# Kernel tuning notes

Hardware: AMD Instinct MI355X
Metric: run time of the kernel (lower is better)

The kernel has to match this reference:

```python
import jax, jax.numpy as jnp
import numpy as np

NEG_SLOPE = 0.2  # PyG GATConv default


def gat_conv(h, src, dst, n_nodes, W, a_src, a_dst, bias, concat):
    """PyG-style GATConv (single linear shared across src/dst, self-loops
    already included in src/dst). W: [heads*out, in]; a_*: [heads, out]."""
    heads, out = a_src.shape
    g = (h @ W.T).reshape(-1, heads, out)  # [N, H, D]
    # per-node attention logits, then gather scalars per edge (PyG order)
    al_src = jnp.einsum('nhd,hd->nh', g, a_src)  # [N, H]
    al_dst = jnp.einsum('nhd,hd->nh', g, a_dst)
    e = jax.nn.leaky_relu(al_src[src] + al_dst[dst], NEG_SLOPE)  # [E, H]
    # segment softmax over incoming edges of each dst node
    e_max = jax.ops.segment_max(e, dst, num_segments=n_nodes)
    e_exp = jnp.exp(e - e_max[dst])
    denom = jax.ops.segment_sum(e_exp, dst, num_segments=n_nodes)
    alpha = e_exp / denom[dst]  # every node has a self-loop -> denom > 0
    msg = g[src] * alpha[..., None]  # [E, H, D]
    out_n = jax.ops.segment_sum(msg, dst, num_segments=n_nodes)  # [N, H, D]
    if concat:
        out_n = out_n.reshape(n_nodes, heads * out)
    else:
        out_n = out_n.mean(axis=1)
    return out_n + bias


def setup_inputs() -> dict:
    key = jax.random.key(0)
    ks = jax.random.split(key, 20)
    N, M = 100000, 1600000
    node_dim, edge_dim, global_dim = 12, 5, 11
    hidden, heads, num_targets = 32, 4, 4
    in1 = node_dim + global_dim  # 23
    s = 0.1
    inp = {
        'x': jax.random.normal(ks[0], (N, node_dim), jnp.float32),
        'edge_index': jax.random.randint(ks[1], (2, M), 0, N, jnp.int32),
        'edge_attr': jax.random.normal(ks[2], (M, edge_dim), jnp.float32),
        'u': jax.random.normal(ks[3], (1, global_dim), jnp.float32),
        # conv1: in1 -> hidden per head, concat
        'W1': jax.random.normal(ks[4], (heads * hidden, in1), jnp.float32) * s,
        'a_src1': jax.random.normal(ks[5], (heads, hidden), jnp.float32) * s,
        'a_dst1': jax.random.normal(ks[6], (heads, hidden), jnp.float32) * s,
        'b1': jnp.zeros((heads * hidden,), jnp.float32),
        # conv2: heads*hidden -> hidden, mean over heads
        'W2': jax.random.normal(ks[7], (heads * hidden, heads * hidden), jnp.float32) * s,
        'a_src2': jax.random.normal(ks[8], (heads, hidden), jnp.float32) * s,
        'a_dst2': jax.random.normal(ks[9], (heads, hidden), jnp.float32) * s,
        'b2': jnp.zeros((hidden,), jnp.float32),
        # decoder: (2*hidden + edge_dim) -> 2*hidden -> hidden -> num_targets
        'dw1': jax.random.normal(ks[10], (2 * hidden, 2 * hidden + edge_dim), jnp.float32) * s,
        'db1': jnp.zeros((2 * hidden,), jnp.float32),
        'dw2': jax.random.normal(ks[11], (hidden, 2 * hidden), jnp.float32) * s,
        'db2': jnp.zeros((hidden,), jnp.float32),
        'dw3': jax.random.normal(ks[12], (num_targets, hidden), jnp.float32) * s,
        'db3': jnp.zeros((num_targets,), jnp.float32),
    }
    return inp


def reference(x, edge_index, edge_attr, u, W1, a_src1, a_dst1, b1,
              W2, a_src2, a_dst2, b2, dw1, db1, dw2, db2, dw3, db3):
    N = x.shape[0]
    loop = jnp.arange(N, dtype=edge_index.dtype)
    src = jnp.concatenate([edge_index[0], loop])  # add self-loops (PyG default)
    dst = jnp.concatenate([edge_index[1], loop])

    u_node = jnp.broadcast_to(u, (N, u.shape[-1]))
    h = jnp.concatenate([x, u_node], axis=-1)  # [N, 23]

    h = jax.nn.elu(gat_conv(h, src, dst, N, W1, a_src1, a_dst1, b1, True))
    h = jax.nn.elu(gat_conv(h, src, dst, N, W2, a_src2, a_dst2, b2, False))

    s0, d0 = edge_index[0], edge_index[1]
    e_in = jnp.concatenate([h[s0], h[d0], edge_attr], axis=-1)  # [M, 69]
    z = jax.nn.relu(e_in @ dw1.T + db1)
    z = jax.nn.relu(z @ dw2.T + db2)
    return z @ dw3.T + db3  # [M, num_targets]
```

## Files before the change

kernel.cpp:

```cpp
#include <hip/hip_runtime.h>

#define DEVINL __device__ __forceinline__

DEVINL float leakyf(float v) { return v > 0.f ? v : 0.2f * v; }
DEVINL float eluf(float v)   { return v > 0.f ? v : __expf(v) - 1.f; }

__global__ void __launch_bounds__(256) k_izero(int* __restrict__ p, int total) {
  int t = blockIdx.x * blockDim.x + threadIdx.x;
  if (t < total) p[t] = 0;
}

__global__ void __launch_bounds__(256) k_count(const int* __restrict__ ei,
                                               int* __restrict__ cnt, int M, int E) {
  int e = blockIdx.x * blockDim.x + threadIdx.x;
  if (e >= E) return;
  int d = (e < M) ? ei[M + e] : e - M;
  atomicAdd(&cnt[d], 1);
}

__global__ void __launch_bounds__(256) k_scan1(const int* __restrict__ cnt,
                                               int* __restrict__ off,
                                               int* __restrict__ bsum, int N) {
  __shared__ int sh[256];
  int i = blockIdx.x * 256 + threadIdx.x;
  int v = (i < N) ? cnt[i] : 0;
  sh[threadIdx.x] = v;
  __syncthreads();
  for (int o = 1; o < 256; o <<= 1) {
    int t = (threadIdx.x >= o) ? sh[threadIdx.x - o] : 0;
    __syncthreads();
    sh[threadIdx.x] += t;
    __syncthreads();
  }
  if (i < N) off[i] = sh[threadIdx.x] - v;
  if (threadIdx.x == 255) bsum[blockIdx.x] = sh[255];
}

__global__ void __launch_bounds__(512) k_scan2(int* __restrict__ bsum, int nb) {
  __shared__ int sh[512];
  int t = threadIdx.x;
  int v = (t < nb) ? bsum[t] : 0;
  sh[t] = v;
  __syncthreads();
  for (int o = 1; o < 512; o <<= 1) {
    int x = (t >= o) ? sh[t - o] : 0;
    __syncthreads();
    sh[t] += x;
    __syncthreads();
  }
  if (t < nb) bsum[t] = sh[t] - v;
}

__global__ void __launch_bounds__(256) k_scan3(int* __restrict__ off,
                                               const int* __restrict__ bsum,
                                               int* __restrict__ cur, int N, int E) {
  int i = blockIdx.x * 256 + threadIdx.x;
  if (i < N) { off[i] += bsum[i >> 8]; cur[i] = 0; }
  if (i == N) off[N] = E;
}

__global__ void __launch_bounds__(256) k_fill(const int* __restrict__ ei,
                                              const int* __restrict__ off,
                                              int* __restrict__ cur,
                                              int* __restrict__ ssrc,
                                              int* __restrict__ idst,
                                              int* __restrict__ ieid, int M, int E) {
  int e = blockIdx.x * blockDim.x + threadIdx.x;
  if (e >= E) return;
  int s, d, id;
  if (e < M) { s = ei[e]; d = ei[M + e]; id = e; }
  else       { s = e - M; d = s; id = -1; }
  int pos = off[d] + atomicAdd(&cur[d], 1);
  ssrc[pos] = s;
  idst[pos] = d;
  ieid[pos] = id;
}

__global__ void k_prep(const float* __restrict__ W1, const float* __restrict__ as1,
                       const float* __restrict__ ad1,
                       const float* __restrict__ W2, const float* __restrict__ as2,
                       const float* __restrict__ ad2,
                       float* __restrict__ wa1s, float* __restrict__ wa1d,
                       float* __restrict__ wa2s, float* __restrict__ wa2d) {
  int t = threadIdx.x;
  if (t < 92) {
    int h = t / 23, c = t % 23;
    float s1 = 0.f, s2 = 0.f;
    for (int dd = 0; dd < 32; ++dd) {
      float w = W1[(h * 32 + dd) * 23 + c];
      s1 += w * as1[h * 32 + dd];
      s2 += w * ad1[h * 32 + dd];
    }
    wa1s[t] = s1;
    wa1d[t] = s2;
  }
  {
    int h = t >> 7, c = t & 127;
    float s1 = 0.f, s2 = 0.f;
    for (int dd = 0; dd < 32; ++dd) {
      float w = W2[(h * 32 + dd) * 128 + c];
      s1 += w * as2[h * 32 + dd];
      s2 += w * ad2[h * 32 + dd];
    }
    wa2s[t] = s1;
    wa2d[t] = s2;
  }
}

__global__ void __launch_bounds__(128) k_g1(
    const float* __restrict__ x, const float* __restrict__ u,
    const float* __restrict__ W1,
    const float* __restrict__ wa1s, const float* __restrict__ wa1d,
    float* __restrict__ g1, float* __restrict__ al1s, float* __restrict__ al1d) {
  int n = blockIdx.x, k = threadIdx.x;
  __shared__ float hs[23];
  if (k < 12) hs[k] = x[n * 12 + k];
  else if (k < 23) hs[k] = u[k - 12];
  __syncthreads();
  const float* w = W1 + k * 23;
  float s = 0.f;
#pragma unroll
  for (int c = 0; c < 23; ++c) s += hs[c] * w[c];
  g1[n * 128 + k] = s;
  if (k < 8) {
    int h = k & 3;
    const float* wa = (k < 4 ? wa1s : wa1d) + h * 23;
    float t = 0.f;
#pragma unroll
    for (int c = 0; c < 23; ++c) t += hs[c] * wa[c];
    (k < 4 ? al1s : al1d)[n * 4 + h] = t;
  }
}

template <int MODE>
__global__ void __launch_bounds__(256) k_gat(
    const float* __restrict__ g, const float* __restrict__ als,
    const float* __restrict__ ald, const int* __restrict__ off,
    const int* __restrict__ ssrc, const float* __restrict__ bias,
    float* __restrict__ outp, int N) {
  int wid = threadIdx.x >> 6, lane = threadIdx.x & 63;
  int d = blockIdx.x * 4 + wid;
  if (d >= N) return;
  int h = lane >> 4;
  float av = ald[d * 4 + h];
  int p0 = off[d], p1 = off[d + 1];
  float accx = 0.f, accy = 0.f, den = 0.f;
  int p = p0;
  for (; p + 4 <= p1; p += 4) {
    int s0 = ssrc[p], s1 = ssrc[p + 1], s2 = ssrc[p + 2], s3 = ssrc[p + 3];
    float l0 = als[s0 * 4 + h], l1 = als[s1 * 4 + h];
    float l2 = als[s2 * 4 + h], l3 = als[s3 * 4 + h];
    float2 G0 = *(const float2*)(g + (size_t)s0 * 128 + 2 * lane);
    float2 G1 = *(const float2*)(g + (size_t)s1 * 128 + 2 * lane);
    float2 G2 = *(const float2*)(g + (size_t)s2 * 128 + 2 * lane);
    float2 G3 = *(const float2*)(g + (size_t)s3 * 128 + 2 * lane);
    float w0 = __expf(leakyf(l0 + av)), w1 = __expf(leakyf(l1 + av));
    float w2 = __expf(leakyf(l2 + av)), w3 = __expf(leakyf(l3 + av));
    accx += w0 * G0.x + w1 * G1.x + w2 * G2.x + w3 * G3.x;
    accy += w0 * G0.y + w1 * G1.y + w2 * G2.y + w3 * G3.y;
    den += (w0 + w1) + (w2 + w3);
  }
  for (; p < p1; ++p) {
    int s = ssrc[p];
    float w = __expf(leakyf(als[s * 4 + h] + av));
    float2 G = *(const float2*)(g + (size_t)s * 128 + 2 * lane);
    accx += w * G.x;
    accy += w * G.y;
    den += w;
  }
  float inv = 1.f / den;
  float vx = accx * inv, vy = accy * inv;
  if (MODE == 0) {
    float2 b = *(const float2*)(bias + 2 * lane);
    float2 o;
    o.x = eluf(vx + b.x);
    o.y = eluf(vy + b.y);
    *(float2*)(outp + (size_t)d * 128 + 2 * lane) = o;
  } else {
    float sx = vx + __shfl_xor(vx, 16);
    sx += __shfl_xor(sx, 32);
    float sy = vy + __shfl_xor(vy, 16);
    sy += __shfl_xor(sy, 32);
    if (lane < 16) {
      float2 o;
      o.x = eluf(0.25f * sx + bias[2 * lane]);
      o.y = eluf(0.25f * sy + bias[2 * lane + 1]);
      *(float2*)(outp + (size_t)d * 32 + 2 * lane) = o;
    }
  }
}

__global__ void __launch_bounds__(128) k_g2t(
    const float* __restrict__ h2, const float* __restrict__ W2,
    const float* __restrict__ wa2s, const float* __restrict__ wa2d,
    float* __restrict__ g2, float* __restrict__ al2s, float* __restrict__ al2d,
    int N, int ntiles) {
  __shared__ float4 w4s[128][32];
  __shared__ float4 hs4[32][32];
  int t = threadIdx.x;

  for (int i = t; i < 4096; i += 128) {
    int c = i >> 5, kk = i & 31;
    float4 v = *(const float4*)(W2 + c * 128 + kk * 4);
    w4s[c][kk ^ ((c >> 2) & 31)] = v;
  }

  int m = t & 31, grp = t >> 5;
  int c0 = 4 * m;

  for (int tile = blockIdx.x; tile < ntiles; tile += gridDim.x) {
    int n0 = tile * 32;
    __syncthreads();
    for (int i = t; i < 1024; i += 128) {
      int n = i >> 5, kk = i & 31;
      int nn = n0 + n;
      hs4[n][kk] = (nn < N) ? *(const float4*)(h2 + (size_t)nn * 128 + kk * 4)
                            : make_float4(0.f, 0.f, 0.f, 0.f);
    }
    __syncthreads();

    float acc[8][4];
#pragma unroll
    for (int n = 0; n < 8; ++n)
#pragma unroll
      for (int j = 0; j < 4; ++j) acc[n][j] = 0.f;

#pragma unroll 8
    for (int kk = 0; kk < 32; ++kk) {
      float4 wj[4];
#pragma unroll
      for (int j = 0; j < 4; ++j) wj[j] = w4s[c0 + j][kk ^ m];
#pragma unroll
      for (int n = 0; n < 8; ++n) {
        float4 hv = hs4[grp * 8 + n][kk];
#pragma unroll
        for (int j = 0; j < 4; ++j) {
          acc[n][j] += hv.x * wj[j].x + hv.y * wj[j].y +
                       hv.z * wj[j].z + hv.w * wj[j].w;
        }
      }
    }
#pragma unroll
    for (int n = 0; n < 8; ++n) {
      int nn = n0 + grp * 8 + n;
      if (nn < N)
        *(float4*)(g2 + (size_t)nn * 128 + c0) =
            make_float4(acc[n][0], acc[n][1], acc[n][2], acc[n][3]);
    }

    for (int v = 0; v < 2; ++v) {
      int idx = t + 128 * v;
      int n = idx >> 3, j = idx & 7, h = j & 3;
      int nn = n0 + n;
      if (nn < N) {
        const float4* wa = (const float4*)((j < 4 ? wa2s : wa2d) + h * 128);
        float s = 0.f;
#pragma unroll
        for (int kk = 0; kk < 32; ++kk) {
          float4 a = hs4[n][kk];
          float4 w = wa[kk];
          s += a.x * w.x + a.y * w.y + a.z * w.z + a.w * w.w;
        }
        (j < 4 ? al2s : al2d)[(size_t)nn * 4 + h] = s;
      }
    }
  }
}

__global__ void __launch_bounds__(256) k_pq(
    const float* __restrict__ h3, const float* __restrict__ dw1,
    float* __restrict__ pq, int N) {
  __shared__ float4 ws4[64][16];
  __shared__ float ht[64][32];
  int t = threadIdx.x;
  for (int i = t; i < 4096; i += 256) {
    int k = i >> 6, c = i & 63;
    ((float*)&ws4[k][(c >> 2) ^ (k & 15)])[c & 3] = dw1[k * 69 + c];
  }
  int n0 = blockIdx.x * 64;
  for (int i = t; i < 2048; i += 256) {
    int n = i >> 5, c = i & 31;
    int nn = n0 + n;
    ht[n][c] = (nn < N) ? h3[(size_t)nn * 32 + c] : 0.f;
  }
  __syncthreads();
  int k2 = t & 127, sub = t >> 7;
  int k = k2 & 63, base4 = (k2 < 64) ? 0 : 8;
  float4 wr[8];
#pragma unroll
  for (int i = 0; i < 8; ++i) wr[i] = ws4[k][(base4 + i) ^ (k & 15)];
  for (int ii = 0; ii < 32; ++ii) {
    int n = sub * 32 + ii;
    const float4* hr = (const float4*)ht[n];
    float s = 0.f;
#pragma unroll
    for (int i = 0; i < 8; ++i) {
      float4 a = hr[i], w = wr[i];
      s += a.x * w.x + a.y * w.y + a.z * w.z + a.w * w.w;
    }
    int nn = n0 + n;
    if (nn < N) pq[(size_t)nn * 128 + k2] = s;
  }
}

__global__ void __launch_bounds__(256) k_dec(
    const float* __restrict__ pq, const int* __restrict__ ssrc,
    const int* __restrict__ idst, const int* __restrict__ ieid,
    const float* __restrict__ ea,
    const float* __restrict__ dw1, const float* __restrict__ db1,
    const float* __restrict__ dw2, const float* __restrict__ db2,
    const float* __restrict__ dw3, const float* __restrict__ db3,
    float* __restrict__ out, int E) {
  __shared__ float4 w2s4[32][16];
  __shared__ float4 ct4[5][16];
  __shared__ float4 b1q[16];
  __shared__ float4 b2q[8];
  __shared__ float4 w3s4[4][8];
  __shared__ float  db3s[4];
  int t = threadIdx.x;
  for (int i = t; i < 512; i += 256) {
    int k = i >> 4, cq = i & 15;
    w2s4[k][cq] = *(const float4*)(dw2 + k * 64 + cq * 4);
  }
  if (t < 80) {
    int c = t / 16, cq = t % 16;
    float4 v;
    v.x = dw1[(4 * cq + 0) * 69 + 64 + c];
    v.y = dw1[(4 * cq + 1) * 69 + 64 + c];
    v.z = dw1[(4 * cq + 2) * 69 + 64 + c];
    v.w = dw1[(4 * cq + 3) * 69 + 64 + c];
    ct4[c][cq] = v;
  } else if (t < 96) {
    b1q[t - 80] = *(const float4*)(db1 + 4 * (t - 80));
  } else if (t < 104) {
    b2q[t - 96] = *(const float4*)(db2 + 4 * (t - 96));
  } else if (t < 136) {
    int o = (t - 104) >> 3, cq = (t - 104) & 7;
    w3s4[o][cq] = *(const float4*)(dw3 + o * 32 + 4 * cq);
  } else if (t < 140) {
    db3s[t - 136] = db3[t - 136];
  }
  __syncthreads();

  int pos0 = blockIdx.x * 512 + t;
  int pos1 = pos0 + 256;
  bool okA = pos0 < E, okB = pos1 < E;
  int pa = okA ? pos0 : 0, pb = okB ? pos1 : 0;
  int eA_ = okA ? ieid[pa] : -1;
  int eB_ = okB ? ieid[pb] : -1;
  bool wA = eA_ >= 0, wB = eB_ >= 0;
  int eidA = wA ? eA_ : 0, eidB = wB ? eB_ : 0;
  int sA = ssrc[pa], dA = idst[pa];
  int sB = ssrc[pb], dB = idst[pb];
  const float4* PA = (const float4*)(pq + (size_t)sA * 128);
  const float4* QA = (const float4*)(pq + (size_t)dA * 128 + 64);
  const float4* PB = (const float4*)(pq + (size_t)sB * 128);
  const float4* QB = (const float4*)(pq + (size_t)dB * 128 + 64);
  const float* eap = ea + (size_t)eidA * 5;
  const float* ebp = ea + (size_t)eidB * 5;
  float eAv[5], eBv[5];
#pragma unroll
  for (int c = 0; c < 5; ++c) { eAv[c] = eap[c]; eBv[c] = ebp[c]; }

  float z2a[32], z2b[32];
#pragma unroll
  for (int kq = 0; kq < 8; ++kq) {
    float4 b = b2q[kq];
    z2a[4 * kq + 0] = b.x; z2a[4 * kq + 1] = b.y;
    z2a[4 * kq + 2] = b.z; z2a[4 * kq + 3] = b.w;
    z2b[4 * kq + 0] = b.x; z2b[4 * kq + 1] = b.y;
    z2b[4 * kq + 2] = b.z; z2b[4 * kq + 3] = b.w;
  }

  for (int cq = 0; cq < 16; ++cq) {
    float4 pA = PA[cq], qA = QA[cq];
    float4 pB = PB[cq], qB = QB[cq];
    float4 bq = b1q[cq];
    float4 zA, zB;
    zA.x = pA.x + qA.x + bq.x; zA.y = pA.y + qA.y + bq.y;
    zA.z = pA.z + qA.z + bq.z; zA.w = pA.w + qA.w + bq.w;
    zB.x = pB.x + qB.x + bq.x; zB.y = pB.y + qB.y + bq.y;
    zB.z = pB.z + qB.z + bq.z; zB.w = pB.w + qB.w + bq.w;
#pragma unroll
    for (int c = 0; c < 5; ++c) {
      float4 cc = ct4[c][cq];
      float ca = eAv[c], cb = eBv[c];
      zA.x += ca * cc.x; zA.y += ca * cc.y; zA.z += ca * cc.z; zA.w += ca * cc.w;
      zB.x += cb * cc.x; zB.y += cb * cc.y; zB.z += cb * cc.z; zB.w += cb * cc.w;
    }
    zA.x = fmaxf(zA.x, 0.f); zA.y = fmaxf(zA.y, 0.f);
    zA.z = fmaxf(zA.z, 0.f); zA.w = fmaxf(zA.w, 0.f);
    zB.x = fmaxf(zB.x, 0.f); zB.y = fmaxf(zB.y, 0.f);
    zB.z = fmaxf(zB.z, 0.f); zB.w = fmaxf(zB.w, 0.f);
#pragma unroll
    for (int k = 0; k < 32; ++k) {
      float4 w = w2s4[k][cq];
      z2a[k] += w.x * zA.x + w.y * zA.y + w.z * zA.z + w.w * zA.w;
      z2b[k] += w.x * zB.x + w.y * zB.y + w.z * zB.z + w.w * zB.w;
    }
  }
#pragma unroll
  for (int k = 0; k < 32; ++k) {
    z2a[k] = fmaxf(z2a[k], 0.f);
    z2b[k] = fmaxf(z2b[k], 0.f);
  }

  float oA[4], oB[4];
#pragma unroll
  for (int o = 0; o < 4; ++o) { oA[o] = db3s[o]; oB[o] = db3s[o]; }
#pragma unroll
  for (int cq = 0; cq < 8; ++cq) {
    float ax = z2a[4 * cq], ay = z2a[4 * cq + 1];
    float az = z2a[4 * cq + 2], aw = z2a[4 * cq + 3];
    float bx = z2b[4 * cq], by = z2b[4 * cq + 1];
    float bz = z2b[4 * cq + 2], bw = z2b[4 * cq + 3];
#pragma unroll
    for (int o = 0; o < 4; ++o) {
      float4 w = w3s4[o][cq];
      oA[o] += ax * w.x + ay * w.y + az * w.z + aw * w.w;
      oB[o] += bx * w.x + by * w.y + bz * w.z + bw * w.w;
    }
  }
  if (wA && okA)
    *(float4*)(out + (size_t)eidA * 4) = make_float4(oA[0], oA[1], oA[2], oA[3]);
  if (wB && okB)
    *(float4*)(out + (size_t)eidB * 4) = make_float4(oB[0], oB[1], oB[2], oB[3]);
}

extern "C" void kernel_launch(void* const* d_in, const int* in_sizes, int n_in,
                              void* d_out, int out_size, void* d_ws, size_t ws_size,
                              hipStream_t stream) {
  const float* x   = (const float*)d_in[0];
  const int*   ei  = (const int*)d_in[1];
  const float* ea  = (const float*)d_in[2];
  const float* u   = (const float*)d_in[3];
  const float* W1  = (const float*)d_in[4];
  const float* as1 = (const float*)d_in[5];
  const float* ad1 = (const float*)d_in[6];
  const float* b1  = (const float*)d_in[7];
  const float* W2  = (const float*)d_in[8];
  const float* as2 = (const float*)d_in[9];
  const float* ad2 = (const float*)d_in[10];
  const float* b2  = (const float*)d_in[11];
  const float* dw1 = (const float*)d_in[12];
  const float* db1 = (const float*)d_in[13];
  const float* dw2 = (const float*)d_in[14];
  const float* db2 = (const float*)d_in[15];
  const float* dw3 = (const float*)d_in[16];
  const float* db3 = (const float*)d_in[17];
  float* out = (float*)d_out;

  const int N = in_sizes[0] / 12;
  const int M = in_sizes[1] / 2;
  const int E = M + N;

  float* ws = (float*)d_ws;
  float* A    = ws;
  float* B    = A + (size_t)N * 128;
  float* H3   = B;
  float* AL1S = B + (size_t)N * 128;
  float* AL1D = AL1S + (size_t)N * 4;
  float* AL2S = AL1D + (size_t)N * 4;
  float* AL2D = AL2S + (size_t)N * 4;
  float* WA1S = AL2D + (size_t)N * 4;
  float* WA1D = WA1S + 96;
  float* WA2S = WA1D + 96;
  float* WA2D = WA2S + 512;
  int* IOFF = (int*)(WA2D + 512);
  int* ICUR = IOFF + (N + 1);
  int* IBS  = ICUR + N;
  int* ISRC = IBS + 512;
  int* IDST = ISRC + E;
  int* IEID = IDST + E;

  int nb = (N + 255) / 256;
  int gE = (E + 255) / 256;

  k_izero<<<nb, 256, 0, stream>>>(ICUR, N);
  k_count<<<gE, 256, 0, stream>>>(ei, ICUR, M, E);
  k_scan1<<<nb, 256, 0, stream>>>(ICUR, IOFF, IBS, N);
  k_scan2<<<1, 512, 0, stream>>>(IBS, nb);
  k_scan3<<<(N + 256) / 256, 256, 0, stream>>>(IOFF, IBS, ICUR, N, E);
  k_fill<<<gE, 256, 0, stream>>>(ei, IOFF, ICUR, ISRC, IDST, IEID, M, E);

  k_prep<<<1, 512, 0, stream>>>(W1, as1, ad1, W2, as2, ad2, WA1S, WA1D, WA2S, WA2D);

  k_g1<<<N, 128, 0, stream>>>(x, u, W1, WA1S, WA1D, A, AL1S, AL1D);
  k_gat<0><<<(N + 3) / 4, 256, 0, stream>>>(A, AL1S, AL1D, IOFF, ISRC, b1, B, N);

  int ntiles = (N + 31) / 32;
  k_g2t<<<512, 128, 0, stream>>>(B, W2, WA2S, WA2D, A, AL2S, AL2D, N, ntiles);
  k_gat<1><<<(N + 3) / 4, 256, 0, stream>>>(A, AL2S, AL2D, IOFF, ISRC, b2, H3, N);

  k_pq<<<(N + 63) / 64, 256, 0, stream>>>(H3, dw1, A, N);
  k_dec<<<(E + 511) / 512, 256, 0, stream>>>(A, ISRC, IDST, IEID, ea, dw1, db1,
                                             dw2, db2, dw3, db3, out, E);
}
```

Before: 1.080 ms.

## Compute source-side decoder projection per edge instead of precomputing per node

The per-node precompute now stores only the destination-side projection (64 floats per node) instead of both source and destination halves. The decoder kernel gathers the raw 32-float source embedding and multiplies it by the first 32 columns of dw1, held in shared memory, for each edge. This halves the random-gather bytes for the source side and the precompute write size. In exchange it adds about 2K FMAs per edge pair plus extra registers, which may lower occupancy.

```diff
diff --git a/kernel.cpp b/kernel.cpp
--- a/kernel.cpp
+++ b/kernel.cpp
@@ -267,15 +267,16 @@
   }
 }
 
-__global__ void __launch_bounds__(256) k_pq(
+__global__ void __launch_bounds__(256) k_q(
     const float* __restrict__ h3, const float* __restrict__ dw1,
-    float* __restrict__ pq, int N) {
-  __shared__ float4 ws4[64][16];
+    float* __restrict__ qt, int N) {
+  __shared__ float4 ws4[64][8];
   __shared__ float ht[64][32];
   int t = threadIdx.x;
-  for (int i = t; i < 4096; i += 256) {
-    int k = i >> 6, c = i & 63;
-    ((float*)&ws4[k][(c >> 2) ^ (k & 15)])[c & 3] = dw1[k * 69 + c];
+  for (int i = t; i < 512; i += 256) {
+    int k = i >> 3, q = i & 7;
+    const float* wp = dw1 + k * 69 + 32 + 4 * q;
+    ws4[k][q] = make_float4(wp[0], wp[1], wp[2], wp[3]);
   }
   int n0 = blockIdx.x * 64;
   for (int i = t; i < 2048; i += 256) {
@@ -284,13 +285,12 @@
     ht[n][c] = (nn < N) ? h3[(size_t)nn * 32 + c] : 0.f;
   }
   __syncthreads();
-  int k2 = t & 127, sub = t >> 7;
-  int k = k2 & 63, base4 = (k2 < 64) ? 0 : 8;
+  int k = t & 63, sub = t >> 6;
   float4 wr[8];
 #pragma unroll
-  for (int i = 0; i < 8; ++i) wr[i] = ws4[k][(base4 + i) ^ (k & 15)];
-  for (int ii = 0; ii < 32; ++ii) {
-    int n = sub * 32 + ii;
+  for (int i = 0; i < 8; ++i) wr[i] = ws4[k][i];
+  for (int ii = 0; ii < 16; ++ii) {
+    int n = sub * 16 + ii;
     const float4* hr = (const float4*)ht[n];
     float s = 0.f;
 #pragma unroll
@@ -299,25 +299,35 @@
       s += a.x * w.x + a.y * w.y + a.z * w.z + a.w * w.w;
     }
     int nn = n0 + n;
-    if (nn < N) pq[(size_t)nn * 128 + k2] = s;
+    if (nn < N) qt[(size_t)nn * 64 + k] = s;
   }
 }
 
 __global__ void __launch_bounds__(256) k_dec(
-    const float* __restrict__ pq, const int* __restrict__ ssrc,
-    const int* __restrict__ idst, const int* __restrict__ ieid,
-    const float* __restrict__ ea,
+    const float* __restrict__ h3, const float* __restrict__ qt,
+    const int* __restrict__ ssrc, const int* __restrict__ idst,
+    const int* __restrict__ ieid, const float* __restrict__ ea,
     const float* __restrict__ dw1, const float* __restrict__ db1,
     const float* __restrict__ dw2, const float* __restrict__ db2,
     const float* __restrict__ dw3, const float* __restrict__ db3,
     float* __restrict__ out, int E) {
+  __shared__ float4 at4[32][16];
+  __shared__ float4 ct4[5][16];
   __shared__ float4 w2s4[32][16];
-  __shared__ float4 ct4[5][16];
   __shared__ float4 b1q[16];
   __shared__ float4 b2q[8];
   __shared__ float4 w3s4[4][8];
   __shared__ float  db3s[4];
   int t = threadIdx.x;
+  for (int i = t; i < 512; i += 256) {
+    int c = i >> 4, cq = i & 15;
+    float4 v;
+    v.x = dw1[(4 * cq + 0) * 69 + c];
+    v.y = dw1[(4 * cq + 1) * 69 + c];
+    v.z = dw1[(4 * cq + 2) * 69 + c];
+    v.w = dw1[(4 * cq + 3) * 69 + c];
+    at4[c][cq] = v;
+  }
   for (int i = t; i < 512; i += 256) {
     int k = i >> 4, cq = i & 15;
     w2s4[k][cq] = *(const float4*)(dw2 + k * 64 + cq * 4);
@@ -352,10 +362,22 @@
   int eidA = wA ? eA_ : 0, eidB = wB ? eB_ : 0;
   int sA = ssrc[pa], dA = idst[pa];
   int sB = ssrc[pb], dB = idst[pb];
-  const float4* PA = (const float4*)(pq + (size_t)sA * 128);
-  const float4* QA = (const float4*)(pq + (size_t)dA * 128 + 64);
-  const float4* PB = (const float4*)(pq + (size_t)sB * 128);
-  const float4* QB = (const float4*)(pq + (size_t)dB * 128 + 64);
+
+  float ha[32], hb[32];
+  {
+    const float4* HA = (const float4*)(h3 + (size_t)sA * 32);
+    const float4* HB = (const float4*)(h3 + (size_t)sB * 32);
+#pragma unroll
+    for (int i = 0; i < 8; ++i) {
+      float4 a = HA[i], b = HB[i];
+      ha[4 * i + 0] = a.x; ha[4 * i + 1] = a.y;
+      ha[4 * i + 2] = a.z; ha[4 * i + 3] = a.w;
+      hb[4 * i + 0] = b.x; hb[4 * i + 1] = b.y;
+      hb[4 * i + 2] = b.z; hb[4 * i + 3] = b.w;
+    }
+  }
+  const float4* QA = (const float4*)(qt + (size_t)dA * 64);
+  const float4* QB = (const float4*)(qt + (size_t)dB * 64);
   const float* eap = ea + (size_t)eidA * 5;
   const float* ebp = ea + (size_t)eidB * 5;
   float eAv[5], eBv[5];
@@ -373,14 +395,20 @@
   }
 
   for (int cq = 0; cq < 16; ++cq) {
-    float4 pA = PA[cq], qA = QA[cq];
-    float4 pB = PB[cq], qB = QB[cq];
+    float4 qA = QA[cq], qB = QB[cq];
     float4 bq = b1q[cq];
     float4 zA, zB;
-    zA.x = pA.x + qA.x + bq.x; zA.y = pA.y + qA.y + bq.y;
-    zA.z = pA.z + qA.z + bq.z; zA.w = pA.w + qA.w + bq.w;
-    zB.x = pB.x + qB.x + bq.x; zB.y = pB.y + qB.y + bq.y;
-    zB.z = pB.z + qB.z + bq.z; zB.w = pB.w + qB.w + bq.w;
+    zA.x = qA.x + bq.x; zA.y = qA.y + bq.y;
+    zA.z = qA.z + bq.z; zA.w = qA.w + bq.w;
+    zB.x = qB.x + bq.x; zB.y = qB.y + bq.y;
+    zB.z = qB.z + bq.z; zB.w = qB.w + bq.w;
+#pragma unroll
+    for (int c = 0; c < 32; ++c) {
+      float4 ac = at4[c][cq];
+      float xa = ha[c], xb = hb[c];
+      zA.x += xa * ac.x; zA.y += xa * ac.y; zA.z += xa * ac.z; zA.w += xa * ac.w;
+      zB.x += xb * ac.x; zB.y += xb * ac.y; zB.z += xb * ac.z; zB.w += xb * ac.w;
+    }
 #pragma unroll
     for (int c = 0; c < 5; ++c) {
       float4 cc = ct4[c][cq];
@@ -492,7 +520,8 @@
   k_g2t<<<512, 128, 0, stream>>>(B, W2, WA2S, WA2D, A, AL2S, AL2D, N, ntiles);
   k_gat<1><<<(N + 3) / 4, 256, 0, stream>>>(A, AL2S, AL2D, IOFF, ISRC, b2, H3, N);
 
-  k_pq<<<(N + 63) / 64, 256, 0, stream>>>(H3, dw1, A, N);
-  k_dec<<<(E + 511) / 512, 256, 0, stream>>>(A, ISRC, IDST, IEID, ea, dw1, db1,
-                                             dw2, db2, dw3, db3, out, E);
-}
+  k_q<<<(N + 63) / 64, 256, 0, stream>>>(H3, dw1, A, N);
+  k_dec<<<(E + 511) / 512, 256, 0, stream>>>(H3, A, ISRC, IDST, IEID, ea,
+                                             dw1, db1, dw2, db2, dw3, db3,
+                                             out, E);
+}
```

Result: slower. 1.137 ms (+5.3%).

## Remap edge decoder to half-wavefront per edge with persistent grid

Applied to the files above, without the earlier changes.

The edge MLP decoder moves from one thread per edge (two edges per thread, with 32-wide accumulators in registers) to 32 lanes per edge. Each lane owns one hidden unit of the second layer and keeps its weight row in registers. The first-layer activations go through shared memory, and the final 4-output projection is reduced with xor shuffles. The launch becomes a fixed 2048-block grid-stride loop. The aim is to coalesce the gathered P/Q row reads and cut per-thread register pressure. The cost is shuffle reductions, extra shared-memory traffic, and only one lane in 32 doing the output store.

```diff
diff --git a/kernel.cpp b/kernel.cpp
--- a/kernel.cpp
+++ b/kernel.cpp
@@ -310,121 +310,70 @@
     const float* __restrict__ dw1, const float* __restrict__ db1,
     const float* __restrict__ dw2, const float* __restrict__ db2,
     const float* __restrict__ dw3, const float* __restrict__ db3,
-    float* __restrict__ out, int E) {
-  __shared__ float4 w2s4[32][16];
-  __shared__ float4 ct4[5][16];
-  __shared__ float4 b1q[16];
-  __shared__ float4 b2q[8];
-  __shared__ float4 w3s4[4][8];
-  __shared__ float  db3s[4];
-  int t = threadIdx.x;
-  for (int i = t; i < 512; i += 256) {
-    int k = i >> 4, cq = i & 15;
-    w2s4[k][cq] = *(const float4*)(dw2 + k * 64 + cq * 4);
-  }
-  if (t < 80) {
-    int c = t / 16, cq = t % 16;
-    float4 v;
-    v.x = dw1[(4 * cq + 0) * 69 + 64 + c];
-    v.y = dw1[(4 * cq + 1) * 69 + 64 + c];
-    v.z = dw1[(4 * cq + 2) * 69 + 64 + c];
-    v.w = dw1[(4 * cq + 3) * 69 + 64 + c];
-    ct4[c][cq] = v;
-  } else if (t < 96) {
-    b1q[t - 80] = *(const float4*)(db1 + 4 * (t - 80));
-  } else if (t < 104) {
-    b2q[t - 96] = *(const float4*)(db2 + 4 * (t - 96));
-  } else if (t < 136) {
-    int o = (t - 104) >> 3, cq = (t - 104) & 7;
-    w3s4[o][cq] = *(const float4*)(dw3 + o * 32 + 4 * cq);
-  } else if (t < 140) {
-    db3s[t - 136] = db3[t - 136];
-  }
-  __syncthreads();
-
-  int pos0 = blockIdx.x * 512 + t;
-  int pos1 = pos0 + 256;
-  bool okA = pos0 < E, okB = pos1 < E;
-  int pa = okA ? pos0 : 0, pb = okB ? pos1 : 0;
-  int eA_ = okA ? ieid[pa] : -1;
-  int eB_ = okB ? ieid[pb] : -1;
-  bool wA = eA_ >= 0, wB = eB_ >= 0;
-  int eidA = wA ? eA_ : 0, eidB = wB ? eB_ : 0;
-  int sA = ssrc[pa], dA = idst[pa];
-  int sB = ssrc[pb], dB = idst[pb];
-  const float4* PA = (const float4*)(pq + (size_t)sA * 128);
-  const float4* QA = (const float4*)(pq + (size_t)dA * 128 + 64);
-  const float4* PB = (const float4*)(pq + (size_t)sB * 128);
-  const float4* QB = (const float4*)(pq + (size_t)dB * 128 + 64);
-  const float* eap = ea + (size_t)eidA * 5;
-  const float* ebp = ea + (size_t)eidB * 5;
-  float eAv[5], eBv[5];
-#pragma unroll
-  for (int c = 0; c < 5; ++c) { eAv[c] = eap[c]; eBv[c] = ebp[c]; }
-
-  float z2a[32], z2b[32];
-#pragma unroll
-  for (int kq = 0; kq < 8; ++kq) {
-    float4 b = b2q[kq];
-    z2a[4 * kq + 0] = b.x; z2a[4 * kq + 1] = b.y;
-    z2a[4 * kq + 2] = b.z; z2a[4 * kq + 3] = b.w;
-    z2b[4 * kq + 0] = b.x; z2b[4 * kq + 1] = b.y;
-    z2b[4 * kq + 2] = b.z; z2b[4 * kq + 3] = b.w;
-  }
-
-  for (int cq = 0; cq < 16; ++cq) {
-    float4 pA = PA[cq], qA = QA[cq];
-    float4 pB = PB[cq], qB = QB[cq];
-    float4 bq = b1q[cq];
-    float4 zA, zB;
-    zA.x = pA.x + qA.x + bq.x; zA.y = pA.y + qA.y + bq.y;
-    zA.z = pA.z + qA.z + bq.z; zA.w = pA.w + qA.w + bq.w;
-    zB.x = pB.x + qB.x + bq.x; zB.y = pB.y + qB.y + bq.y;
-    zB.z = pB.z + qB.z + bq.z; zB.w = pB.w + qB.w + bq.w;
-#pragma unroll
-    for (int c = 0; c < 5; ++c) {
-      float4 cc = ct4[c][cq];
-      float ca = eAv[c], cb = eBv[c];
-      zA.x += ca * cc.x; zA.y += ca * cc.y; zA.z += ca * cc.z; zA.w += ca * cc.w;
-      zB.x += cb * cc.x; zB.y += cb * cc.y; zB.z += cb * cc.z; zB.w += cb * cc.w;
-    }
-    zA.x = fmaxf(zA.x, 0.f); zA.y = fmaxf(zA.y, 0.f);
-    zA.z = fmaxf(zA.z, 0.f); zA.w = fmaxf(zA.w, 0.f);
-    zB.x = fmaxf(zB.x, 0.f); zB.y = fmaxf(zB.y, 0.f);
-    zB.z = fmaxf(zB.z, 0.f); zB.w = fmaxf(zB.w, 0.f);
-#pragma unroll
-    for (int k = 0; k < 32; ++k) {
-      float4 w = w2s4[k][cq];
-      z2a[k] += w.x * zA.x + w.y * zA.y + w.z * zA.z + w.w * zA.w;
-      z2b[k] += w.x * zB.x + w.y * zB.y + w.z * zB.z + w.w * zB.w;
-    }
-  }
-#pragma unroll
-  for (int k = 0; k < 32; ++k) {
-    z2a[k] = fmaxf(z2a[k], 0.f);
-    z2b[k] = fmaxf(z2b[k], 0.f);
-  }
-
-  float oA[4], oB[4];
-#pragma unroll
-  for (int o = 0; o < 4; ++o) { oA[o] = db3s[o]; oB[o] = db3s[o]; }
-#pragma unroll
-  for (int cq = 0; cq < 8; ++cq) {
-    float ax = z2a[4 * cq], ay = z2a[4 * cq + 1];
-    float az = z2a[4 * cq + 2], aw = z2a[4 * cq + 3];
-    float bx = z2b[4 * cq], by = z2b[4 * cq + 1];
-    float bz = z2b[4 * cq + 2], bw = z2b[4 * cq + 3];
-#pragma unroll
-    for (int o = 0; o < 4; ++o) {
-      float4 w = w3s4[o][cq];
-      oA[o] += ax * w.x + ay * w.y + az * w.z + aw * w.w;
-      oB[o] += bx * w.x + by * w.y + bz * w.z + bw * w.w;
-    }
-  }
-  if (wA && okA)
-    *(float4*)(out + (size_t)eidA * 4) = make_float4(oA[0], oA[1], oA[2], oA[3]);
-  if (wB && okB)
-    *(float4*)(out + (size_t)eidB * 4) = make_float4(oB[0], oB[1], oB[2], oB[3]);
+    float* __restrict__ out, int E, int npairs) {
+  __shared__ float z1s[4][128];
+  int wv = threadIdx.x >> 6, lane = threadIdx.x & 63;
+  int half = lane >> 5;
+  int k = lane & 31;
+
+  float4 wrow[16];
+#pragma unroll
+  for (int i = 0; i < 16; ++i)
+    wrow[i] = *(const float4*)(dw2 + k * 64 + 4 * i);
+  float w3r0 = dw3[k], w3r1 = dw3[32 + k], w3r2 = dw3[64 + k], w3r3 = dw3[96 + k];
+  float b1a = db1[2 * k], b1b = db1[2 * k + 1];
+  float ct0a = dw1[(2 * k) * 69 + 64], ct0b = dw1[(2 * k + 1) * 69 + 64];
+  float ct1a = dw1[(2 * k) * 69 + 65], ct1b = dw1[(2 * k + 1) * 69 + 65];
+  float ct2a = dw1[(2 * k) * 69 + 66], ct2b = dw1[(2 * k + 1) * 69 + 66];
+  float ct3a = dw1[(2 * k) * 69 + 67], ct3b = dw1[(2 * k + 1) * 69 + 67];
+  float ct4a = dw1[(2 * k) * 69 + 68], ct4b = dw1[(2 * k + 1) * 69 + 68];
+  float b2k = db2[k];
+  float d30 = db3[0], d31 = db3[1], d32 = db3[2], d33 = db3[3];
+
+  float* zme = &z1s[wv][half * 64];
+
+  int stride = gridDim.x * 4;
+  for (int pr = blockIdx.x * 4 + wv; pr < npairs; pr += stride) {
+    int pos = pr * 2 + half;
+    bool ok = pos < E;
+    int pp = ok ? pos : 0;
+    int eid = ok ? ieid[pp] : -1;
+    int s = ssrc[pp], d = idst[pp];
+
+    float2 Pv = *(const float2*)(pq + (size_t)s * 128 + 2 * k);
+    float2 Qv = *(const float2*)(pq + (size_t)d * 128 + 64 + 2 * k);
+    const float* ep = ea + (size_t)(eid < 0 ? 0 : eid) * 5;
+    float e0 = ep[0], e1 = ep[1], e2 = ep[2], e3 = ep[3], e4 = ep[4];
+
+    float za = Pv.x + Qv.x + b1a +
+               ct0a * e0 + ct1a * e1 + ct2a * e2 + ct3a * e3 + ct4a * e4;
+    float zb = Pv.y + Qv.y + b1b +
+               ct0b * e0 + ct1b * e1 + ct2b * e2 + ct3b * e3 + ct4b * e4;
+    za = fmaxf(za, 0.f);
+    zb = fmaxf(zb, 0.f);
+    *(float2*)(zme + 2 * k) = make_float2(za, zb);
+
+    float z2 = b2k;
+#pragma unroll
+    for (int cq = 0; cq < 16; ++cq) {
+      float4 z = *(const float4*)(zme + 4 * cq);
+      float4 w = wrow[cq];
+      z2 += z.x * w.x + z.y * w.y + z.z * w.z + z.w * w.w;
+    }
+    z2 = fmaxf(z2, 0.f);
+
+    float p0 = z2 * w3r0, p1 = z2 * w3r1, p2 = z2 * w3r2, p3 = z2 * w3r3;
+#pragma unroll
+    for (int m = 16; m >= 1; m >>= 1) {
+      p0 += __shfl_xor(p0, m);
+      p1 += __shfl_xor(p1, m);
+      p2 += __shfl_xor(p2, m);
+      p3 += __shfl_xor(p3, m);
+    }
+    if (k == 0 && eid >= 0)
+      *(float4*)(out + (size_t)eid * 4) =
+          make_float4(p0 + d30, p1 + d31, p2 + d32, p3 + d33);
+  }
 }
 
 extern "C" void kernel_launch(void* const* d_in, const int* in_sizes, int n_in,
@@ -493,6 +442,7 @@
   k_gat<1><<<(N + 3) / 4, 256, 0, stream>>>(A, AL2S, AL2D, IOFF, ISRC, b2, H3, N);
 
   k_pq<<<(N + 63) / 64, 256, 0, stream>>>(H3, dw1, A, N);
-  k_dec<<<(E + 511) / 512, 256, 0, stream>>>(A, ISRC, IDST, IEID, ea, dw1, db1,
-                                             dw2, db2, dw3, db3, out, E);
-}
+  int npairs = (E + 1) / 2;
+  k_dec<<<2048, 256, 0, stream>>>(A, ISRC, IDST, IEID, ea, dw1, db1,
+                                  dw2, db2, dw3, db3, out, E, npairs);
+}
```

After: 1.230 ms. 1.14x slower.
